# Kernel tuning notes

Measured on AMD Instinct MI355X. Metric: run time of the kernel, lower is better.

Reference implementation:

```python
import jax, jax.numpy as jnp
import numpy as np

B, N, T = 128, 64, 20
I_CNN, H, E, L, NCLS, V = 24, 128, 300, 256, 100, 96


def _coords():
    # make_coords(64): 8x8 grid, grid = [(i - W//2)/W, (j - W//2)/W]
    W = 8
    g = (np.arange(W) - W // 2) / W
    c = np.stack(np.meshgrid(g, g, indexing='ij'), -1).reshape(W * W, 2)
    return jnp.asarray(c, jnp.float32)


def _lstm_final_c(seq, lens, w_ih, w_hh, b_ih, b_hh):
    # seq: [B,T,E]; returns cell state at each sequence's true length (packed-LSTM semantics)
    Bd = seq.shape[0]
    mask = (jnp.arange(T)[None, :] < lens[:, None]).astype(seq.dtype)  # [B,T]

    def step(carry, inp):
        h, c = carry
        x_t, m = inp  # [B,E], [B,1]
        gates = x_t @ w_ih.T + b_ih + h @ w_hh.T + b_hh  # [B,4H], torch gate order i,f,g,o
        i_g, f_g, g_g, o_g = jnp.split(gates, 4, axis=-1)
        c_new = jax.nn.sigmoid(f_g) * c + jax.nn.sigmoid(i_g) * jnp.tanh(g_g)
        h_new = jax.nn.sigmoid(o_g) * jnp.tanh(c_new)
        c = m * c_new + (1.0 - m) * c
        h = m * h_new + (1.0 - m) * h
        return (h, c), None

    h0 = jnp.zeros((Bd, H), seq.dtype)
    (_, cT), _ = jax.lax.scan(step, (h0, h0), (seq.transpose(1, 0, 2), mask.T[:, :, None]))
    return cT


def _forward(box_feats, emb, w_ih, w_hh, b_ih, b_hh,
             g_w1, g_b1, g_w2, g_b2, g_w3, g_b3, g_w4, g_b4,
             f_w1, f_b1, f_w2, f_b2, f_w3, f_b3, q_feats, q_lens):
    tok = jnp.tanh(emb[q_feats])  # [B,T,E]
    q_rnn = _lstm_final_c(tok, q_lens, w_ih, w_hh, b_ih, b_hh)  # [B,H]
    coords = jnp.broadcast_to(_coords()[None], (B, N, 2))
    box = jnp.concatenate([box_feats, coords], -1)  # [B,N,26]
    D = box.shape[-1]
    b_i = jnp.broadcast_to(box[:, :, None, :], (B, N, N, D))
    b_j = jnp.broadcast_to(box[:, None, :, :], (B, N, N, D))
    qst = jnp.broadcast_to(q_rnn[:, None, None, :], (B, N, N, H))
    b_full = jnp.concatenate([b_i, b_j, qst], -1).reshape(B * N * N, 2 * D + H)  # [B*N*N,180]
    x = jax.nn.relu(b_full @ g_w1 + g_b1)
    x = jax.nn.relu(x @ g_w2 + g_b2)
    x = jax.nn.relu(x @ g_w3 + g_b3)
    x = jax.nn.relu(x @ g_w4 + g_b4)
    g_out = x.reshape(B, N * N, L).sum(1)  # [B,256]
    y = jax.nn.relu(g_out @ f_w1 + f_b1)
    y = jax.nn.relu(y @ f_w2 + f_b2)
    return y @ f_w3 + f_b3  # [B,NCLS]  (dropout is identity at inference)


def setup_inputs() -> dict:
    key = jax.random.key(0)
    ks = jax.random.split(key, 16)

    def w(k, shape, s=0.05):
        return jax.random.normal(k, shape, jnp.float32) * s

    Din = 2 * (I_CNN + 2) + H  # 180
    z = lambda n: jnp.zeros((n,), jnp.float32)
    return dict(
        box_feats=jax.random.normal(ks[0], (B, N, I_CNN), jnp.float32),
        emb=w(ks[1], (V, E), 0.1),
        w_ih=w(ks[2], (4 * H, E)), w_hh=w(ks[3], (4 * H, H)),
        b_ih=z(4 * H), b_hh=z(4 * H),
        g_w1=w(ks[4], (Din, L)), g_b1=z(L),
        g_w2=w(ks[5], (L, L)), g_b2=z(L),
        g_w3=w(ks[6], (L, L)), g_b3=z(L),
        g_w4=w(ks[7], (L, L)), g_b4=z(L),
        f_w1=w(ks[8], (L, L)), f_b1=z(L),
        f_w2=w(ks[9], (L, L)), f_b2=z(L),
        f_w3=w(ks[10], (L, NCLS)), f_b3=z(NCLS),
        q_feats=jax.random.randint(ks[11], (B, T), 0, V),
        q_lens=jax.random.randint(ks[12], (B,), 1, T + 1),
    )


def reference(box_feats, emb, w_ih, w_hh, b_ih, b_hh,
              g_w1, g_b1, g_w2, g_b2, g_w3, g_b3, g_w4, g_b4,
              f_w1, f_b1, f_w2, f_b2, f_w3, f_b3, q_feats, q_lens):
    return _forward(box_feats, emb, w_ih, w_hh, b_ih, b_hh,
                    g_w1, g_b1, g_w2, g_b2, g_w3, g_b3, g_w4, g_b4,
                    f_w1, f_b1, f_w2, f_b2, f_w3, f_b3, q_feats, q_lens)
```

## Files before the change

kernel.cpp:

```cpp
#include <hip/hip_runtime.h>
#include <hip/hip_bf16.h>

typedef unsigned int uint;
typedef unsigned short ushort;
typedef __attribute__((ext_vector_type(8))) short bf16x8;
typedef __attribute__((ext_vector_type(4))) float f32x4;

__device__ __forceinline__ float bf2f(ushort u) {
    return __uint_as_float(((uint)u) << 16);
}
__device__ __forceinline__ ushort f2bf(float f) {
    uint u = __float_as_uint(f);
    u += 0x7FFFu + ((u >> 16) & 1u);
    return (ushort)(u >> 16);
}
__device__ __forceinline__ uint cvtpk(float lo, float hi) {
    uint r;
    asm("v_cvt_pk_bf16_f32 %0, %1, %2" : "=v"(r) : "v"(lo), "v"(hi));
    return r;
}
__device__ __forceinline__ float sigm(float x) {
    return 1.0f / (1.0f + expf(-x));
}

__global__ __launch_bounds__(512) void kPW(
    const float* __restrict__ emb, const float* __restrict__ w_ih,
    const float* __restrict__ b_ih, float* __restrict__ P,
    const float* __restrict__ g_w2, const float* __restrict__ g_w3,
    const float* __restrict__ g_w4, ushort* __restrict__ Wst)
{
    int tid = threadIdx.x;
    if (blockIdx.x < 96) {
        __shared__ __align__(16) float te[300];
        int v = blockIdx.x;
        for (int k = tid; k < 300; k += 512) te[k] = tanhf(emb[v * 300 + k]);
        __syncthreads();
        int g = tid;
        float acc = b_ih[g];
        const float4* wr = (const float4*)(w_ih + g * 300);
        const float4* tv = (const float4*)te;
        for (int k = 0; k < 75; ++k) {
            float4 w4 = wr[k], t4 = tv[k];
            acc += w4.x * t4.x + w4.y * t4.y + w4.z * t4.z + w4.w * t4.w;
        }
        P[v * 512 + g] = acc;
    } else if (tid < 256) {
        int blk = blockIdx.x - 96;
        int li = blk >> 3, kc = blk & 7, col = tid;
        const float* W = (li == 0) ? g_w2 : (li == 1) ? g_w3 : g_w4;
        ushort* dst = Wst + li * 65536 + kc * 8192
                    + (col >> 4) * 512 + (col & 15) * 8;
        for (int kk = 0; kk < 32; ++kk)
            dst[(kk >> 3) * 128 + (kk & 7)] = f2bf(W[(kc * 32 + kk) * 256 + col]);
    }
}

#define WROW 132
__global__ __launch_bounds__(512) void kLA(
    const float* __restrict__ P, const float* __restrict__ w_hh,
    const float* __restrict__ b_hh, const float* __restrict__ g_w1,
    const float* __restrict__ g_b1, const int* __restrict__ q_feats,
    const int* __restrict__ q_lens, const float* __restrict__ box_feats,
    ushort* __restrict__ A1, ushort* __restrict__ A2)
{
    __shared__ __align__(16) ushort whh[512 * WROW];
    __shared__ __align__(16) float h[128];
    __shared__ __align__(16) float c[128];
    __shared__ float gates[512];
    __shared__ float wq2[2][256];
    __shared__ float box[64][26];
    int b = blockIdx.x, tid = threadIdx.x;
    if (tid < 128) { h[tid] = 0.f; c[tid] = 0.f; }
    for (int i = tid * 4; i < 65536; i += 2048) {
        int g = i >> 7, k = i & 127;
        float4 w4 = *(const float4*)&w_hh[i];
        uint2 o;
        o.x = cvtpk(w4.x, w4.y);
        o.y = cvtpk(w4.z, w4.w);
        *(uint2*)&whh[g * WROW + k] = o;
    }
    for (int idx = tid; idx < 64 * 26; idx += 512) {
        int n = idx / 26, d = idx - n * 26;
        float v;
        if (d < 24)       v = box_feats[(b * 64 + n) * 24 + d];
        else if (d == 24) v = ((n >> 3) - 4) * 0.125f;
        else              v = ((n & 7) - 4) * 0.125f;
        box[n][d] = v;
    }
    __syncthreads();
    int len = q_lens[b];
    const int g = tid;
    const ushort* wr = &whh[g * WROW];
    for (int t = 0; t < len; ++t) {
        int idx = q_feats[b * 20 + t];
        float acc = P[idx * 512 + g] + b_hh[g];
        #pragma unroll
        for (int k8 = 0; k8 < 16; ++k8) {
            uint2 wlo = *(const uint2*)&wr[k8 * 8];
            uint2 whi = *(const uint2*)&wr[k8 * 8 + 4];
            float4 h0 = *(const float4*)&h[k8 * 8];
            float4 h1 = *(const float4*)&h[k8 * 8 + 4];
            acc += bf2f((ushort)(wlo.x & 0xFFFFu)) * h0.x
                 + bf2f((ushort)(wlo.x >> 16))     * h0.y
                 + bf2f((ushort)(wlo.y & 0xFFFFu)) * h0.z
                 + bf2f((ushort)(wlo.y >> 16))     * h0.w
                 + bf2f((ushort)(whi.x & 0xFFFFu)) * h1.x
                 + bf2f((ushort)(whi.x >> 16))     * h1.y
                 + bf2f((ushort)(whi.y & 0xFFFFu)) * h1.z
                 + bf2f((ushort)(whi.y >> 16))     * h1.w;
        }
        gates[g] = acc;
        __syncthreads();
        if (tid < 128) {
            float ig = sigm(gates[tid]);
            float fg = sigm(gates[128 + tid]);
            float gg = tanhf(gates[256 + tid]);
            float og = sigm(gates[384 + tid]);
            float cn = fg * c[tid] + ig * gg;
            c[tid] = cn;
            h[tid] = og * tanhf(cn);
        }
        __syncthreads();
    }
    {
        int l = tid & 255, half = tid >> 8;
        float acc = (half == 0) ? g_b1[l] : 0.f;
        for (int k = 0; k < 64; ++k)
            acc += c[half * 64 + k] * g_w1[(52 + half * 64 + k) * 256 + l];
        wq2[half][l] = acc;
    }
    __syncthreads();
    {
        int l = tid & 255, n0 = tid >> 8;
        float w1a[26], w1b[26];
        #pragma unroll
        for (int d = 0; d < 26; ++d) {
            w1a[d] = g_w1[d * 256 + l];
            w1b[d] = g_w1[(26 + d) * 256 + l];
        }
        float wqv = wq2[0][l] + wq2[1][l];
        for (int n = n0; n < 64; n += 2) {
            float a1 = 0.f, a2 = wqv;
            #pragma unroll
            for (int d = 0; d < 26; ++d) {
                a1 += box[n][d] * w1a[d];
                a2 += box[n][d] * w1b[d];
            }
            A1[(b * 64 + n) * 256 + l] = f2bf(a1);
            A2[(b * 64 + n) * 256 + l] = f2bf(a2);
        }
    }
}

#define MFMA1(wa, xb, a) __builtin_amdgcn_mfma_f32_16x16x32_bf16(wa, xb, a, 0, 0, 0)

__global__ __launch_bounds__(256, 4) void kD(
    const ushort* __restrict__ A1, const ushort* __restrict__ A2,
    const ushort* __restrict__ Wst,
    const float* __restrict__ b2, const float* __restrict__ b3,
    const float* __restrict__ b4, float* __restrict__ partial)
{
    __shared__ __align__(16) ushort lds_x[64 * 256];

    const int tid = threadIdx.x;
    const int bi = blockIdx.x, b = bi >> 6;
    const int lane = tid & 63, wv = tid >> 6;
    const int l15 = lane & 15, lg = lane >> 4;
    const int col0 = wv * 64;

    const int l0 = (tid & 31) << 3;
    bf16x8 a1v = *(const bf16x8*)&A1[bi * 256 + l0];

    const ushort* A2b = A2 + b * 64 * 256;
    #pragma unroll
    for (int it = 0; it < 8; ++it) {
        int row = it * 8 + (tid >> 5);
        uint4 v = *(const uint4*)(A2b + row * 256 + l0);
        uint vv[4] = {v.x, v.y, v.z, v.w}, ov[4];
        #pragma unroll
        for (int qq = 0; qq < 4; ++qq) {
            float f0 = bf2f((ushort)a1v[2 * qq])     + bf2f((ushort)(vv[qq] & 0xFFFFu));
            float f1 = bf2f((ushort)a1v[2 * qq + 1]) + bf2f((ushort)(vv[qq] >> 16));
            ov[qq] = cvtpk(fmaxf(f0, 0.f), fmaxf(f1, 0.f));
        }
        *(uint4*)&lds_x[row * 256 + (l0 ^ ((row & 7) << 3))] =
            make_uint4(ov[0], ov[1], ov[2], ov[3]);
    }
    __syncthreads();

    const char* wbase = (const char*)Wst + (col0 >> 4) * 1024 + lane * 16;

    #pragma unroll 1
    for (int li = 0; li < 3; ++li) {
        f32x4 acc[4][4];
        #pragma unroll
        for (int rt = 0; rt < 4; ++rt)
            #pragma unroll
            for (int ct = 0; ct < 4; ++ct)
                acc[rt][ct] = (f32x4){0.f, 0.f, 0.f, 0.f};

        #pragma unroll 1
        for (int kc = 0; kc < 8; ++kc) {
            const char* wp = wbase + li * 131072 + kc * 16384;
            bf16x8 wa0 = *(const bf16x8*)(wp);
            bf16x8 wa1 = *(const bf16x8*)(wp + 1024);
            bf16x8 wa2 = *(const bf16x8*)(wp + 2048);
            bf16x8 wa3 = *(const bf16x8*)(wp + 3072);
            bf16x8 xb[4];
            #pragma unroll
            for (int rt = 0; rt < 4; ++rt) {
                int row = rt * 16 + l15;
                xb[rt] = *(const bf16x8*)
                    &lds_x[row * 256 + ((kc * 32 + lg * 8) ^ ((row & 7) << 3))];
            }
            __builtin_amdgcn_s_setprio(1);
            #pragma unroll
            for (int rt = 0; rt < 4; ++rt) {
                acc[rt][0] = MFMA1(wa0, xb[rt], acc[rt][0]);
                acc[rt][1] = MFMA1(wa1, xb[rt], acc[rt][1]);
                acc[rt][2] = MFMA1(wa2, xb[rt], acc[rt][2]);
                acc[rt][3] = MFMA1(wa3, xb[rt], acc[rt][3]);
            }
            __builtin_amdgcn_s_setprio(0);
        }

        const float* bias = (li == 0) ? b2 : (li == 1) ? b3 : b4;
        f32x4 bv0 = *(const f32x4*)(bias + col0 + lg * 4);
        f32x4 bv1 = *(const f32x4*)(bias + col0 + 16 + lg * 4);
        f32x4 bv2 = *(const f32x4*)(bias + col0 + 32 + lg * 4);
        f32x4 bv3 = *(const f32x4*)(bias + col0 + 48 + lg * 4);

        if (li < 2) {
            __builtin_amdgcn_s_barrier();
            #pragma unroll
            for (int rt = 0; rt < 4; ++rt) {
                int row = rt * 16 + l15;
                int sw = (row & 7) << 3;
                #pragma unroll
                for (int ct = 0; ct < 4; ++ct) {
                    f32x4 a = acc[rt][ct];
                    f32x4 bv = (ct == 0) ? bv0 : (ct == 1) ? bv1 : (ct == 2) ? bv2 : bv3;
                    uint2 pk;
                    pk.x = cvtpk(fmaxf(a[0] + bv[0], 0.f), fmaxf(a[1] + bv[1], 0.f));
                    pk.y = cvtpk(fmaxf(a[2] + bv[2], 0.f), fmaxf(a[3] + bv[3], 0.f));
                    *(uint2*)&lds_x[row * 256 + ((col0 + ct * 16 + lg * 4) ^ sw)] = pk;
                }
            }
            asm volatile("s_waitcnt lgkmcnt(0)" ::: "memory");
            __builtin_amdgcn_sched_barrier(0);
            __builtin_amdgcn_s_barrier();
        } else {
            #pragma unroll
            for (int ct = 0; ct < 4; ++ct) {
                f32x4 bv = (ct == 0) ? bv0 : (ct == 1) ? bv1 : (ct == 2) ? bv2 : bv3;
                f32x4 s = {0.f, 0.f, 0.f, 0.f};
                #pragma unroll
                for (int rt = 0; rt < 4; ++rt) {
                    f32x4 a = acc[rt][ct];
                    s[0] += fmaxf(a[0] + bv[0], 0.f);
                    s[1] += fmaxf(a[1] + bv[1], 0.f);
                    s[2] += fmaxf(a[2] + bv[2], 0.f);
                    s[3] += fmaxf(a[3] + bv[3], 0.f);
                }
                #pragma unroll
                for (int m = 1; m < 16; m <<= 1) {
                    #pragma unroll
                    for (int r = 0; r < 4; ++r) s[r] += __shfl_xor(s[r], m, 64);
                }
                if (l15 == 0) {
                    float4 o = {s[0], s[1], s[2], s[3]};
                    *(float4*)&partial[bi * 256 + col0 + ct * 16 + lg * 4] = o;
                }
            }
        }
    }
}

__global__ __launch_bounds__(256) void kRF(
    const float* __restrict__ partial,
    const float* __restrict__ f_w1, const float* __restrict__ f_b1,
    const float* __restrict__ f_w2, const float* __restrict__ f_b2,
    const float* __restrict__ f_w3, const float* __restrict__ f_b3,
    float* __restrict__ out)
{
    __shared__ float g[256], y1[256], y2[256];
    int b = blockIdx.x, t = threadIdx.x;
    {
        float s = 0.f;
        const float* pb = partial + b * 64 * 256 + t;
        #pragma unroll 8
        for (int i = 0; i < 64; ++i) s += pb[i * 256];
        g[t] = s;
    }
    __syncthreads();
    float acc = f_b1[t];
    for (int k = 0; k < 256; ++k) acc += g[k] * f_w1[k * 256 + t];
    y1[t] = fmaxf(acc, 0.f);
    __syncthreads();
    acc = f_b2[t];
    for (int k = 0; k < 256; ++k) acc += y1[k] * f_w2[k * 256 + t];
    y2[t] = fmaxf(acc, 0.f);
    __syncthreads();
    if (t < 100) {
        float o = f_b3[t];
        for (int k = 0; k < 256; ++k) o += y2[k] * f_w3[k * 100 + t];
        out[b * 100 + t] = o;
    }
}

extern "C" void kernel_launch(void* const* d_in, const int* in_sizes, int n_in,
                              void* d_out, int out_size, void* d_ws, size_t ws_size,
                              hipStream_t stream)
{
    const float* box_feats = (const float*)d_in[0];
    const float* emb   = (const float*)d_in[1];
    const float* w_ih  = (const float*)d_in[2];
    const float* w_hh  = (const float*)d_in[3];
    const float* b_ih  = (const float*)d_in[4];
    const float* b_hh  = (const float*)d_in[5];
    const float* g_w1  = (const float*)d_in[6];
    const float* g_b1  = (const float*)d_in[7];
    const float* g_w2  = (const float*)d_in[8];
    const float* g_b2  = (const float*)d_in[9];
    const float* g_w3  = (const float*)d_in[10];
    const float* g_b3  = (const float*)d_in[11];
    const float* g_w4  = (const float*)d_in[12];
    const float* g_b4  = (const float*)d_in[13];
    const float* f_w1  = (const float*)d_in[14];
    const float* f_b1  = (const float*)d_in[15];
    const float* f_w2  = (const float*)d_in[16];
    const float* f_b2  = (const float*)d_in[17];
    const float* f_w3  = (const float*)d_in[18];
    const float* f_b3  = (const float*)d_in[19];
    const int* q_feats = (const int*)d_in[20];
    const int* q_lens  = (const int*)d_in[21];
    float* out = (float*)d_out;

    char* ws = (char*)d_ws;
    float*  P    = (float*) (ws + 0);
    ushort* A1   = (ushort*)(ws + 196608);
    ushort* A2   = (ushort*)(ws + 4390912);
    ushort* Wst  = (ushort*)(ws + 8585216);
    float*  part = (float*) (ws + 8978432);

    hipLaunchKernelGGL(kPW, dim3(120),  dim3(512), 0, stream,
                       emb, w_ih, b_ih, P, g_w2, g_w3, g_w4, Wst);
    hipLaunchKernelGGL(kLA, dim3(128),  dim3(512), 0, stream,
                       P, w_hh, b_hh, g_w1, g_b1, q_feats, q_lens, box_feats, A1, A2);
    hipLaunchKernelGGL(kD,  dim3(8192), dim3(256), 0, stream,
                       A1, A2, Wst, g_b2, g_b3, g_b4, part);
    hipLaunchKernelGGL(kRF, dim3(128),  dim3(256), 0, stream,
                       part, f_w1, f_b1, f_w2, f_b2, f_w3, f_b3, out);
}
```

Before: 290.5 us.

## Switch main MLP GEMMs to 32x32x16 MFMA and split accumulation chains

```diff
diff --git a/kernel.cpp b/kernel.cpp
--- a/kernel.cpp
+++ b/kernel.cpp
@@ -5,6 +5,7 @@
 typedef unsigned short ushort;
 typedef __attribute__((ext_vector_type(8))) short bf16x8;
 typedef __attribute__((ext_vector_type(4))) float f32x4;
+typedef __attribute__((ext_vector_type(16))) float f32x16;
 
 __device__ __forceinline__ float bf2f(ushort u) {
     return __uint_as_float(((uint)u) << 16);
@@ -48,10 +49,17 @@
         int blk = blockIdx.x - 96;
         int li = blk >> 3, kc = blk & 7, col = tid;
         const float* W = (li == 0) ? g_w2 : (li == 1) ? g_w3 : g_w4;
-        ushort* dst = Wst + li * 65536 + kc * 8192
-                    + (col >> 4) * 512 + (col & 15) * 8;
-        for (int kk = 0; kk < 32; ++kk)
-            dst[(kk >> 3) * 128 + (kk & 7)] = f2bf(W[(kc * 32 + kk) * 256 + col]);
+        int cg = col >> 5, c31 = col & 31;
+        #pragma unroll
+        for (int ks2 = 0; ks2 < 2; ++ks2) {
+            int ks16 = kc * 2 + ks2;
+            ushort* dst = Wst + li * 65536 + ks16 * 4096 + cg * 512 + c31 * 8;
+            #pragma unroll
+            for (int e = 0; e < 2; ++e)
+                #pragma unroll
+                for (int j = 0; j < 8; ++j)
+                    dst[e * 256 + j] = f2bf(W[(ks16 * 16 + e * 8 + j) * 256 + col]);
+        }
     }
 }
 
@@ -93,23 +101,25 @@
     const ushort* wr = &whh[g * WROW];
     for (int t = 0; t < len; ++t) {
         int idx = q_feats[b * 20 + t];
-        float acc = P[idx * 512 + g] + b_hh[g];
+        float acc0 = P[idx * 512 + g] + b_hh[g];
+        float acc1 = 0.f;
         #pragma unroll
         for (int k8 = 0; k8 < 16; ++k8) {
             uint2 wlo = *(const uint2*)&wr[k8 * 8];
             uint2 whi = *(const uint2*)&wr[k8 * 8 + 4];
             float4 h0 = *(const float4*)&h[k8 * 8];
             float4 h1 = *(const float4*)&h[k8 * 8 + 4];
-            acc += bf2f((ushort)(wlo.x & 0xFFFFu)) * h0.x
-                 + bf2f((ushort)(wlo.x >> 16))     * h0.y
-                 + bf2f((ushort)(wlo.y & 0xFFFFu)) * h0.z
-                 + bf2f((ushort)(wlo.y >> 16))     * h0.w
-                 + bf2f((ushort)(whi.x & 0xFFFFu)) * h1.x
-                 + bf2f((ushort)(whi.x >> 16))     * h1.y
-                 + bf2f((ushort)(whi.y & 0xFFFFu)) * h1.z
-                 + bf2f((ushort)(whi.y >> 16))     * h1.w;
-        }
-        gates[g] = acc;
+            float s0 = bf2f((ushort)(wlo.x & 0xFFFFu)) * h0.x
+                     + bf2f((ushort)(wlo.x >> 16))     * h0.y
+                     + bf2f((ushort)(wlo.y & 0xFFFFu)) * h0.z
+                     + bf2f((ushort)(wlo.y >> 16))     * h0.w;
+            float s1 = bf2f((ushort)(whi.x & 0xFFFFu)) * h1.x
+                     + bf2f((ushort)(whi.x >> 16))     * h1.y
+                     + bf2f((ushort)(whi.y & 0xFFFFu)) * h1.z
+                     + bf2f((ushort)(whi.y >> 16))     * h1.w;
+            if (k8 & 1) acc1 += s0 + s1; else acc0 += s0 + s1;
+        }
+        gates[g] = acc0 + acc1;
         __syncthreads();
         if (tid < 128) {
             float ig = sigm(gates[tid]);
@@ -152,7 +162,7 @@
     }
 }
 
-#define MFMA1(wa, xb, a) __builtin_amdgcn_mfma_f32_16x16x32_bf16(wa, xb, a, 0, 0, 0)
+#define MFMA32(wa, xb, a) __builtin_amdgcn_mfma_f32_32x32x16_bf16(wa, xb, a, 0, 0, 0)
 
 __global__ __launch_bounds__(256, 4) void kD(
     const ushort* __restrict__ A1, const ushort* __restrict__ A2,
@@ -165,8 +175,9 @@
     const int tid = threadIdx.x;
     const int bi = blockIdx.x, b = bi >> 6;
     const int lane = tid & 63, wv = tid >> 6;
-    const int l15 = lane & 15, lg = lane >> 4;
+    const int l31 = lane & 31, e8 = lane >> 5;
     const int col0 = wv * 64;
+    const int rsw = (l31 & 7) << 3;
 
     const int l0 = (tid & 31) << 3;
     bf16x8 a1v = *(const bf16x8*)&A1[bi * 256 + l0];
@@ -188,62 +199,67 @@
     }
     __syncthreads();
 
-    const char* wbase = (const char*)Wst + (col0 >> 4) * 1024 + lane * 16;
+    const char* wbase = (const char*)Wst + (wv * 2) * 1024 + e8 * 512 + l31 * 16;
 
     #pragma unroll 1
     for (int li = 0; li < 3; ++li) {
-        f32x4 acc[4][4];
-        #pragma unroll
-        for (int rt = 0; rt < 4; ++rt)
-            #pragma unroll
-            for (int ct = 0; ct < 4; ++ct)
-                acc[rt][ct] = (f32x4){0.f, 0.f, 0.f, 0.f};
+        f32x16 acc00, acc01, acc10, acc11;
+        #pragma unroll
+        for (int r = 0; r < 16; ++r) {
+            acc00[r] = 0.f; acc01[r] = 0.f; acc10[r] = 0.f; acc11[r] = 0.f;
+        }
 
         #pragma unroll 1
         for (int kc = 0; kc < 8; ++kc) {
-            const char* wp = wbase + li * 131072 + kc * 16384;
-            bf16x8 wa0 = *(const bf16x8*)(wp);
-            bf16x8 wa1 = *(const bf16x8*)(wp + 1024);
-            bf16x8 wa2 = *(const bf16x8*)(wp + 2048);
-            bf16x8 wa3 = *(const bf16x8*)(wp + 3072);
-            bf16x8 xb[4];
-            #pragma unroll
-            for (int rt = 0; rt < 4; ++rt) {
-                int row = rt * 16 + l15;
-                xb[rt] = *(const bf16x8*)
-                    &lds_x[row * 256 + ((kc * 32 + lg * 8) ^ ((row & 7) << 3))];
+            #pragma unroll
+            for (int ks = 0; ks < 2; ++ks) {
+                const char* wp = wbase + li * 131072 + (kc * 2 + ks) * 8192;
+                bf16x8 wa0 = *(const bf16x8*)(wp);
+                bf16x8 wa1 = *(const bf16x8*)(wp + 1024);
+                int g0 = kc * 4 + ks * 2 + e8;
+                int r0 = l31, r1 = 32 + l31;
+                bf16x8 xb0 = *(const bf16x8*)
+                    &lds_x[r0 * 256 + ((g0 << 3) ^ rsw)];
+                bf16x8 xb1 = *(const bf16x8*)
+                    &lds_x[r1 * 256 + ((g0 << 3) ^ rsw)];
+                __builtin_amdgcn_s_setprio(1);
+                acc00 = MFMA32(wa0, xb0, acc00);
+                acc01 = MFMA32(wa1, xb0, acc01);
+                acc10 = MFMA32(wa0, xb1, acc10);
+                acc11 = MFMA32(wa1, xb1, acc11);
+                __builtin_amdgcn_s_setprio(0);
             }
-            __builtin_amdgcn_s_setprio(1);
-            #pragma unroll
-            for (int rt = 0; rt < 4; ++rt) {
-                acc[rt][0] = MFMA1(wa0, xb[rt], acc[rt][0]);
-                acc[rt][1] = MFMA1(wa1, xb[rt], acc[rt][1]);
-                acc[rt][2] = MFMA1(wa2, xb[rt], acc[rt][2]);
-                acc[rt][3] = MFMA1(wa3, xb[rt], acc[rt][3]);
-            }
-            __builtin_amdgcn_s_setprio(0);
         }
 
         const float* bias = (li == 0) ? b2 : (li == 1) ? b3 : b4;
-        f32x4 bv0 = *(const f32x4*)(bias + col0 + lg * 4);
-        f32x4 bv1 = *(const f32x4*)(bias + col0 + 16 + lg * 4);
-        f32x4 bv2 = *(const f32x4*)(bias + col0 + 32 + lg * 4);
-        f32x4 bv3 = *(const f32x4*)(bias + col0 + 48 + lg * 4);
+        f32x4 bv[2][4];
+        #pragma unroll
+        for (int ct = 0; ct < 2; ++ct)
+            #pragma unroll
+            for (int r4 = 0; r4 < 4; ++r4)
+                bv[ct][r4] = *(const f32x4*)(bias + col0 + ct * 32 + r4 * 8 + 4 * e8);
 
         if (li < 2) {
             __builtin_amdgcn_s_barrier();
             #pragma unroll
-            for (int rt = 0; rt < 4; ++rt) {
-                int row = rt * 16 + l15;
-                int sw = (row & 7) << 3;
+            for (int rt = 0; rt < 2; ++rt) {
+                int row = rt * 32 + l31;
                 #pragma unroll
-                for (int ct = 0; ct < 4; ++ct) {
-                    f32x4 a = acc[rt][ct];
-                    f32x4 bv = (ct == 0) ? bv0 : (ct == 1) ? bv1 : (ct == 2) ? bv2 : bv3;
-                    uint2 pk;
-                    pk.x = cvtpk(fmaxf(a[0] + bv[0], 0.f), fmaxf(a[1] + bv[1], 0.f));
-                    pk.y = cvtpk(fmaxf(a[2] + bv[2], 0.f), fmaxf(a[3] + bv[3], 0.f));
-                    *(uint2*)&lds_x[row * 256 + ((col0 + ct * 16 + lg * 4) ^ sw)] = pk;
+                for (int ct = 0; ct < 2; ++ct) {
+                    f32x16 a = (rt == 0) ? (ct == 0 ? acc00 : acc01)
+                                         : (ct == 0 ? acc10 : acc11);
+                    #pragma unroll
+                    for (int r4 = 0; r4 < 4; ++r4) {
+                        f32x4 bq = bv[ct][r4];
+                        int cb = col0 + ct * 32 + r4 * 8 + 4 * e8;
+                        int el = (cb & 7) | ((((cb >> 3) ^ (row & 7))) << 3);
+                        uint2 pk;
+                        pk.x = cvtpk(fmaxf(a[4 * r4 + 0] + bq[0], 0.f),
+                                     fmaxf(a[4 * r4 + 1] + bq[1], 0.f));
+                        pk.y = cvtpk(fmaxf(a[4 * r4 + 2] + bq[2], 0.f),
+                                     fmaxf(a[4 * r4 + 3] + bq[3], 0.f));
+                        *(uint2*)&lds_x[row * 256 + el] = pk;
+                    }
                 }
             }
             asm volatile("s_waitcnt lgkmcnt(0)" ::: "memory");
@@ -251,25 +267,28 @@
             __builtin_amdgcn_s_barrier();
         } else {
             #pragma unroll
-            for (int ct = 0; ct < 4; ++ct) {
-                f32x4 bv = (ct == 0) ? bv0 : (ct == 1) ? bv1 : (ct == 2) ? bv2 : bv3;
-                f32x4 s = {0.f, 0.f, 0.f, 0.f};
+            for (int ct = 0; ct < 2; ++ct) {
+                float s[16];
                 #pragma unroll
-                for (int rt = 0; rt < 4; ++rt) {
-                    f32x4 a = acc[rt][ct];
-                    s[0] += fmaxf(a[0] + bv[0], 0.f);
-                    s[1] += fmaxf(a[1] + bv[1], 0.f);
-                    s[2] += fmaxf(a[2] + bv[2], 0.f);
-                    s[3] += fmaxf(a[3] + bv[3], 0.f);
+                for (int r = 0; r < 16; ++r) {
+                    float bq = bv[ct][r >> 2][r & 3];
+                    float v0 = (ct == 0) ? acc00[r] : acc01[r];
+                    float v1 = (ct == 0) ? acc10[r] : acc11[r];
+                    s[r] = fmaxf(v0 + bq, 0.f) + fmaxf(v1 + bq, 0.f);
                 }
                 #pragma unroll
-                for (int m = 1; m < 16; m <<= 1) {
+                for (int m = 1; m < 32; m <<= 1)
                     #pragma unroll
-                    for (int r = 0; r < 4; ++r) s[r] += __shfl_xor(s[r], m, 64);
-                }
-                if (l15 == 0) {
-                    float4 o = {s[0], s[1], s[2], s[3]};
-                    *(float4*)&partial[bi * 256 + col0 + ct * 16 + lg * 4] = o;
+                    for (int r = 0; r < 16; ++r)
+                        s[r] += __shfl_xor(s[r], m, 64);
+                if (l31 == 0) {
+                    #pragma unroll
+                    for (int r4 = 0; r4 < 4; ++r4) {
+                        float4 o = {s[4 * r4 + 0], s[4 * r4 + 1],
+                                    s[4 * r4 + 2], s[4 * r4 + 3]};
+                        *(float4*)&partial[bi * 256 + col0 + ct * 32
+                                           + r4 * 8 + 4 * e8] = o;
+                    }
                 }
             }
         }
@@ -286,25 +305,45 @@
     __shared__ float g[256], y1[256], y2[256];
     int b = blockIdx.x, t = threadIdx.x;
     {
-        float s = 0.f;
+        float s0 = 0.f, s1 = 0.f;
         const float* pb = partial + b * 64 * 256 + t;
         #pragma unroll 8
-        for (int i = 0; i < 64; ++i) s += pb[i * 256];
-        g[t] = s;
-    }
-    __syncthreads();
-    float acc = f_b1[t];
-    for (int k = 0; k < 256; ++k) acc += g[k] * f_w1[k * 256 + t];
-    y1[t] = fmaxf(acc, 0.f);
-    __syncthreads();
-    acc = f_b2[t];
-    for (int k = 0; k < 256; ++k) acc += y1[k] * f_w2[k * 256 + t];
-    y2[t] = fmaxf(acc, 0.f);
+        for (int i = 0; i < 64; i += 2) { s0 += pb[i * 256]; s1 += pb[(i + 1) * 256]; }
+        g[t] = s0 + s1;
+    }
+    __syncthreads();
+    {
+        float a0 = 0.f, a1 = 0.f, a2 = 0.f, a3 = 0.f;
+        #pragma unroll 4
+        for (int k = 0; k < 256; k += 4) {
+            a0 += g[k]     * f_w1[(k)     * 256 + t];
+            a1 += g[k + 1] * f_w1[(k + 1) * 256 + t];
+            a2 += g[k + 2] * f_w1[(k + 2) * 256 + t];
+            a3 += g[k + 3] * f_w1[(k + 3) * 256 + t];
+        }
+        y1[t] = fmaxf(f_b1[t] + (a0 + a1) + (a2 + a3), 0.f);
+    }
+    __syncthreads();
+    {
+        float a0 = 0.f, a1 = 0.f, a2 = 0.f, a3 = 0.f;
+        #pragma unroll 4
+        for (int k = 0; k < 256; k += 4) {
+            a0 += y1[k]     * f_w2[(k)     * 256 + t];
+            a1 += y1[k + 1] * f_w2[(k + 1) * 256 + t];
+            a2 += y1[k + 2] * f_w2[(k + 2) * 256 + t];
+            a3 += y1[k + 3] * f_w2[(k + 3) * 256 + t];
+        }
+        y2[t] = fmaxf(f_b2[t] + (a0 + a1) + (a2 + a3), 0.f);
+    }
     __syncthreads();
     if (t < 100) {
-        float o = f_b3[t];
-        for (int k = 0; k < 256; ++k) o += y2[k] * f_w3[k * 100 + t];
-        out[b * 100 + t] = o;
+        float a0 = 0.f, a1 = 0.f;
+        #pragma unroll 4
+        for (int k = 0; k < 256; k += 2) {
+            a0 += y2[k]     * f_w3[(k)     * 100 + t];
+            a1 += y2[k + 1] * f_w3[(k + 1) * 100 + t];
+        }
+        out[b * 100 + t] = f_b3[t] + a0 + a1;
     }
 }
 
```

Measured after the change: 357.5 us. 23.1% more time.
